# Kernel tuning notes

Hardware: AMD Instinct MI355X
Metric: run time of the kernel (lower is better)

## Reference

```python
import jax, jax.numpy as jnp
from jax import lax
import numpy as np

INPUT_SIZE = 512
HIDDEN_SIZE = 1024
OUTPUT_SIZE = 128
B, T = 64, 512


def setup_inputs() -> dict:
    key = jax.random.key(0)
    ks = jax.random.split(key, 7)
    s = 1.0 / np.sqrt(HIDDEN_SIZE)  # PyTorch LSTM init scale
    x = jax.random.normal(ks[0], (B, T, INPUT_SIZE), dtype=jnp.float32)
    W_ih = jax.random.uniform(ks[1], (4 * HIDDEN_SIZE, INPUT_SIZE), jnp.float32, -s, s)
    W_hh = jax.random.uniform(ks[2], (4 * HIDDEN_SIZE, HIDDEN_SIZE), jnp.float32, -s, s)
    b_ih = jax.random.uniform(ks[3], (4 * HIDDEN_SIZE,), jnp.float32, -s, s)
    b_hh = jax.random.uniform(ks[4], (4 * HIDDEN_SIZE,), jnp.float32, -s, s)
    W_clf = jax.random.uniform(ks[5], (OUTPUT_SIZE, HIDDEN_SIZE), jnp.float32, -s, s)
    b_clf = jax.random.uniform(ks[6], (OUTPUT_SIZE,), jnp.float32, -s, s)
    return {"x": x, "W_ih": W_ih, "W_hh": W_hh, "b_ih": b_ih,
            "b_hh": b_hh, "W_clf": W_clf, "b_clf": b_clf}


def reference(x, W_ih, W_hh, b_ih, b_hh, W_clf, b_clf):
    # Single-layer unidirectional LSTM, PyTorch gate order (i, f, g, o).
    # recurrent_dropout p=0.0 -> identity, omitted.
    Bsz = x.shape[0]
    H = W_hh.shape[1]
    h0 = jnp.zeros((Bsz, H), dtype=x.dtype)
    c0 = jnp.zeros((Bsz, H), dtype=x.dtype)
    b = b_ih + b_hh

    def step(carry, xt):
        h, c = carry
        gates = xt @ W_ih.T + h @ W_hh.T + b  # [B, 4H]
        i, f, g, o = jnp.split(gates, 4, axis=-1)
        c = jax.nn.sigmoid(f) * c + jax.nn.sigmoid(i) * jnp.tanh(g)
        h = jax.nn.sigmoid(o) * jnp.tanh(c)
        return (h, c), None

    (h_last, _), _ = lax.scan(step, (h0, c0), jnp.swapaxes(x, 0, 1))  # scan over T
    return h_last @ W_clf.T + b_clf  # [B, output_size]
```

## Files before the change

### kernel.cpp

```cpp
#include <hip/hip_runtime.h>

#define TSEQ 512
#define BATCH 64
#define INS 512
#define HID 1024
#define NOUT 128
#define NWG 256
#define NTHR 256
#define SLOT_HALFS 65536
#define BG_HALFS 32768
#define FLAGS_BYTES 32768
#define XH_OFF ((size_t)32768)
#define XH_HALFS (2ull * TSEQ * 16384)
#define WIHB_OFF (XH_OFF + XH_HALFS * 2)
#define WIHB_HALFS (128ull * 16384)
#define WHHB_OFF (WIHB_OFF + WIHB_HALFS * 2)
#define WHHB_HALFS (128ull * 32768)
#define HB_OFF_PRE (WHHB_OFF + WHHB_HALFS * 2)

typedef _Float16 half8 __attribute__((ext_vector_type(8)));
typedef float f32x4 __attribute__((ext_vector_type(4)));

__device__ __forceinline__ float sigf(float v) {
  return __builtin_amdgcn_rcpf(1.0f + __expf(-v));
}
__device__ __forceinline__ float tanh_fast(float v) {
  float e = __expf(2.0f * fabsf(v));
  float t = 1.0f - 2.0f * __builtin_amdgcn_rcpf(e + 1.0f);
  return copysignf(t, v);
}
__device__ __forceinline__ half8 cvt8(const float* p) {
  float4 lo = *(const float4*)p, hi = *(const float4*)(p + 4);
  return half8{(_Float16)lo.x, (_Float16)lo.y, (_Float16)lo.z, (_Float16)lo.w,
               (_Float16)hi.x, (_Float16)hi.y, (_Float16)hi.z, (_Float16)hi.w};
}
__device__ __forceinline__ void gload_lds16(const void* g, void* l) {
  __builtin_amdgcn_global_load_lds(
      (const __attribute__((address_space(1))) unsigned int*)g,
      (__attribute__((address_space(3))) unsigned int*)l, 16, 0, 0);
}

__global__ __launch_bounds__(NTHR, 1) void lstm_persist(
    const float* __restrict__ x, const float* __restrict__ W_ih,
    const float* __restrict__ W_hh, const float* __restrict__ b_ih,
    const float* __restrict__ b_hh, const float* __restrict__ W_clf,
    const float* __restrict__ b_clf, float* __restrict__ out,
    void* ws, int nbuf, int use_pre, int do_fence) {
  __shared__ __align__(16) char smem[65536];
  _Float16* hs = (_Float16*)smem;
  float* gates = (float*)smem;

  const int tid = threadIdx.x;
  const int wg = blockIdx.x;
  const int bg = wg >> 7;
  const int cgrp = wg & 127;
  const int wv = tid >> 6;
  const int mi = wv >> 1;
  const int ni = wv & 1;
  const int lane = tid & 63;
  const int nn = lane & 15;
  const int kq = lane >> 4;

  unsigned* flags = (unsigned*)ws;
  _Float16* xh = (_Float16*)((char*)ws + XH_OFF);
  _Float16* wihb = (_Float16*)((char*)ws + WIHB_OFF);
  _Float16* whhb = (_Float16*)((char*)ws + WHHB_OFF);
  _Float16* hb = (_Float16*)((char*)ws + (use_pre ? HB_OFF_PRE : (size_t)FLAGS_BYTES));

  __builtin_amdgcn_fence(__ATOMIC_ACQUIRE, "agent");

  const int c_l = 16 * ni + nn;
  const int ncol = (c_l >> 3) * HID + 8 * cgrp + (c_l & 7);

  if (use_pre) {
    const int gtid = wg * NTHR + tid;
    for (unsigned u = gtid; u < 2097152u; u += NWG * NTHR) {
      int ko = u & 63, t = (u >> 6) & (TSEQ - 1), b = u >> 15;
      half8 v = cvt8(x + ((size_t)b * TSEQ + t) * INS + ko * 8);
      size_t d = ((size_t)((b >> 5) * TSEQ + t) << 14) +
                 (size_t)(((((b >> 4) & 1) * 16 + (ko >> 2)) * 512) +
                          ((ko & 3) * 16 + (b & 15)) * 8);
      *(half8*)(xh + d) = v;
    }
    for (unsigned u = gtid; u < 262144u; u += NWG * NTHR) {
      int le = u & 63, kc = (u >> 6) & 15, nie = (u >> 10) & 1, cge = u >> 11;
      int c = nie * 16 + (le & 15);
      int nc = (c >> 3) * HID + 8 * cge + (c & 7);
      half8 v = cvt8(W_ih + (size_t)nc * INS + kc * 32 + (le >> 4) * 8);
      *(half8*)(wihb + (((size_t)cge << 14) + (size_t)((nie * 16 + kc) * 512 + le * 8))) = v;
    }
    for (unsigned u = gtid; u < 524288u; u += NWG * NTHR) {
      int le = u & 63, kc = (u >> 6) & 31, nie = (u >> 11) & 1, cge = u >> 12;
      int c = nie * 16 + (le & 15);
      int nc = (c >> 3) * HID + 8 * cge + (c & 7);
      half8 v = cvt8(W_hh + (size_t)nc * HID + kc * 32 + (le >> 4) * 8);
      *(half8*)(whhb + (((size_t)cge << 15) + (size_t)((nie * 32 + kc) * 512 + le * 8))) = v;
    }
    __builtin_amdgcn_fence(__ATOMIC_RELEASE, "agent");
  }

  const int dl = tid & 7, blp = tid >> 3;
  const int dgl = 8 * cgrp + dl;
  const float bI = b_ih[dgl] + b_hh[dgl];
  const float bF = b_ih[HID + dgl] + b_hh[HID + dgl];
  const float bG = b_ih[2 * HID + dgl] + b_hh[2 * HID + dgl];
  const float bO = b_ih[3 * HID + dgl] + b_hh[3 * HID + dgl];

  __syncthreads();
  if (tid == 0)
    __hip_atomic_store(flags + wg, 1u, __ATOMIC_RELAXED, __HIP_MEMORY_SCOPE_AGENT);
  {
    int ok;
    do {
      unsigned v = __hip_atomic_load(flags + tid, __ATOMIC_RELAXED,
                                     __HIP_MEMORY_SCOPE_AGENT);
      ok = (v >= 1u);
      if (!ok) __builtin_amdgcn_s_sleep(1);
    } while (!__syncthreads_and(ok));
  }
  __builtin_amdgcn_fence(__ATOMIC_ACQUIRE, "workgroup");

  auto xpart = [&](int t) -> f32x4 {
    f32x4 a0 = {0.f, 0.f, 0.f, 0.f}, a1 = {0.f, 0.f, 0.f, 0.f};
    if (use_pre) {
      const _Float16* xb = xh + ((size_t)(bg * TSEQ + t) << 14) + mi * 16 * 512 + lane * 8;
      const _Float16* wb = wihb + ((size_t)cgrp << 14) + ni * 16 * 512 + lane * 8;
#pragma unroll
      for (int kc = 0; kc < 16; kc += 2) {
        half8 A0 = *(const half8*)(xb + kc * 512);
        half8 B0 = *(const half8*)(wb + kc * 512);
        half8 A1 = *(const half8*)(xb + (kc + 1) * 512);
        half8 B1 = *(const half8*)(wb + (kc + 1) * 512);
        a0 = __builtin_amdgcn_mfma_f32_16x16x32_f16(A0, B0, a0, 0, 0, 0);
        a1 = __builtin_amdgcn_mfma_f32_16x16x32_f16(A1, B1, a1, 0, 0, 0);
      }
    } else {
      const float* xr = x + ((size_t)(32 * bg + 16 * mi + nn) * TSEQ + t) * INS + kq * 8;
      const float* wr = W_ih + (size_t)ncol * INS + kq * 8;
#pragma unroll
      for (int kc = 0; kc < 16; kc += 2) {
        half8 A0 = cvt8(xr + kc * 32), B0 = cvt8(wr + kc * 32);
        half8 A1 = cvt8(xr + (kc + 1) * 32), B1 = cvt8(wr + (kc + 1) * 32);
        a0 = __builtin_amdgcn_mfma_f32_16x16x32_f16(A0, B0, a0, 0, 0, 0);
        a1 = __builtin_amdgcn_mfma_f32_16x16x32_f16(A1, B1, a1, 0, 0, 0);
      }
    }
    return a0 + a1;
  };

  f32x4 accx = xpart(0);
  float c_state = 0.f;
  int sr = 0;

  for (int t = 0; t < TSEQ; ++t) {
    int sw = sr + 1; if (sw == nbuf) sw = 0;

    {
      const _Float16* hsrc = hb + (size_t)sr * SLOT_HALFS + (size_t)bg * BG_HALFS +
                             wv * 8192 + lane * 8;
      char* ldst = smem + (size_t)wv * 16384;
#pragma unroll
      for (int i = 0; i < 16; ++i)
        gload_lds16(hsrc + i * 512, ldst + i * 1024);
    }
    __syncthreads();

    f32x4 a0 = accx, a1 = {0.f, 0.f, 0.f, 0.f};
    {
      const _Float16* wc = whhb + ((size_t)cgrp << 15) + ni * 32 * 512 + lane * 8;
      const _Float16* ab = hs + mi * 32 * 512 + lane * 8;
#pragma unroll
      for (int kc = 0; kc < 32; kc += 2) {
        half8 A0 = *(const half8*)(ab + kc * 512);
        half8 B0 = *(const half8*)(wc + kc * 512);
        half8 A1 = *(const half8*)(ab + (kc + 1) * 512);
        half8 B1 = *(const half8*)(wc + (kc + 1) * 512);
        a0 = __builtin_amdgcn_mfma_f32_16x16x32_f16(A0, B0, a0, 0, 0, 0);
        a1 = __builtin_amdgcn_mfma_f32_16x16x32_f16(A1, B1, a1, 0, 0, 0);
      }
    }
    f32x4 acc = a0 + a1;
    __syncthreads();

    {
      int gx = c_l >> 3, dx = c_l & 7, bx = mi * 16 + kq * 4;
#pragma unroll
      for (int r = 0; r < 4; ++r) gates[(gx * 32 + bx + r) * 9 + dx] = acc[r];
    }
    __syncthreads();

    float xi = gates[(0 * 32 + blp) * 9 + dl] + bI;
    float xf = gates[(1 * 32 + blp) * 9 + dl] + bF;
    float xg = gates[(2 * 32 + blp) * 9 + dl] + bG;
    float xo = gates[(3 * 32 + blp) * 9 + dl] + bO;
    float cn = sigf(xf) * c_state + sigf(xi) * tanh_fast(xg);
    c_state = cn;
    float hv = sigf(xo) * tanh_fast(cn);

    {
      unsigned hw = (unsigned)__builtin_bit_cast(unsigned short, (_Float16)hv);
      unsigned o1 = __shfl_down(hw, 1), o2 = __shfl_down(hw, 2), o3 = __shfl_down(hw, 3);
      if ((dl & 3) == 0) {
        unsigned lo = hw | (o1 << 16), hi2 = o2 | (o3 << 16);
        unsigned long long u = ((unsigned long long)hi2 << 32) | lo;
        _Float16* hd = hb + (size_t)sw * SLOT_HALFS + (size_t)bg * BG_HALFS;
        size_t idx = (size_t)(((blp >> 4) * 32 + (cgrp >> 2)) * 512) +
                     (size_t)(((cgrp & 3) * 16 + (blp & 15)) * 8 + (dl & 4));
        __hip_atomic_store((unsigned long long*)(hd + idx), u, __ATOMIC_RELAXED,
                           __HIP_MEMORY_SCOPE_AGENT);
      }
    }

    __syncthreads();
    if (tid == 0)
      __hip_atomic_store(flags + wg, (unsigned)(t + 2), __ATOMIC_RELAXED,
                         __HIP_MEMORY_SCOPE_AGENT);

    int tn = t + 1 < TSEQ ? t + 1 : t;
    accx = xpart(tn);

    {
      const unsigned T = (unsigned)(t + 2);
      int ok;
      do {
        int okl = 1;
        if (tid < 128) {
          unsigned v = __hip_atomic_load(flags + bg * 128 + tid, __ATOMIC_RELAXED,
                                         __HIP_MEMORY_SCOPE_AGENT);
          okl = (v >= T);
        }
        ok = okl;
        if (!ok) __builtin_amdgcn_s_sleep(1);
      } while (!__syncthreads_and(ok));
    }
    __builtin_amdgcn_fence(__ATOMIC_ACQUIRE, "workgroup");
    if (do_fence) __builtin_amdgcn_fence(__ATOMIC_ACQUIRE, "agent");
    sr = sw;
  }

  {
    const _Float16* hf = hb + (size_t)sr * SLOT_HALFS + (size_t)bg * BG_HALFS;
    int bl = cgrp >> 2;
    int b = 32 * bg + bl;
    int o = (cgrp & 3) * 32 + (tid >> 3);
    int ks = tid & 7;
    int mif = bl >> 4, ml = bl & 15;
    const float* wr = W_clf + (size_t)o * HID;
    float s = 0.f;
    for (int i = 0; i < 128; ++i) {
      size_t idx = (size_t)((mif * 32 + (i >> 2)) * 512) +
                   (size_t)(((i & 3) * 16 + ml) * 8 + ks);
      s += (float)hf[idx] * wr[8 * i + ks];
    }
    s += __shfl_down(s, 4, 8);
    s += __shfl_down(s, 2, 8);
    s += __shfl_down(s, 1, 8);
    if (ks == 0) out[b * NOUT + o] = s + b_clf[o];
  }
}

extern "C" void kernel_launch(void* const* d_in, const int* in_sizes, int n_in,
                              void* d_out, int out_size, void* d_ws, size_t ws_size,
                              hipStream_t stream) {
  const float* x = (const float*)d_in[0];
  const float* W_ih = (const float*)d_in[1];
  const float* W_hh = (const float*)d_in[2];
  const float* b_ih = (const float*)d_in[3];
  const float* b_hh = (const float*)d_in[4];
  const float* W_clf = (const float*)d_in[5];
  const float* b_clf = (const float*)d_in[6];
  float* out = (float*)d_out;

  int use_pre = (ws_size >= HB_OFF_PRE + 2ull * SLOT_HALFS * 2) ? 1 : 0;
  size_t hb_off = use_pre ? HB_OFF_PRE : (size_t)FLAGS_BYTES;
  int nbuf = (ws_size >= hb_off + 129ull * SLOT_HALFS * 2) ? 129 : 2;
  int do_fence = (nbuf == 2) ? 1 : 0;

  hipMemsetAsync(d_ws, 0, FLAGS_BYTES, stream);
  hipMemsetAsync((char*)d_ws + hb_off, 0, SLOT_HALFS * 2, stream);

  void* args[] = {(void*)&x,    (void*)&W_ih,  (void*)&W_hh,   (void*)&b_ih,
                  (void*)&b_hh, (void*)&W_clf, (void*)&b_clf,  (void*)&out,
                  (void*)&d_ws, (void*)&nbuf,  (void*)&use_pre, (void*)&do_fence};
  hipLaunchCooperativeKernel((const void*)lstm_persist, dim3(NWG), dim3(NTHR),
                             args, 0, stream);
}
```

Baseline: 2.343 ms.

## Interleave gate columns so LSTM cell update runs in registers via bpermute

```diff
diff --git a/kernel.cpp b/kernel.cpp
--- a/kernel.cpp
+++ b/kernel.cpp
@@ -39,6 +39,10 @@
       (const __attribute__((address_space(1))) unsigned int*)g,
       (__attribute__((address_space(3))) unsigned int*)l, 16, 0, 0);
 }
+__device__ __forceinline__ float bperm_f(int byteaddr, float v) {
+  return __builtin_bit_cast(
+      float, __builtin_amdgcn_ds_bpermute(byteaddr, __builtin_bit_cast(int, v)));
+}
 
 __global__ __launch_bounds__(NTHR, 1) void lstm_persist(
     const float* __restrict__ x, const float* __restrict__ W_ih,
@@ -48,7 +52,6 @@
     void* ws, int nbuf, int use_pre, int do_fence) {
   __shared__ __align__(16) char smem[65536];
   _Float16* hs = (_Float16*)smem;
-  float* gates = (float*)smem;
 
   const int tid = threadIdx.x;
   const int wg = blockIdx.x;
@@ -70,7 +73,9 @@
   __builtin_amdgcn_fence(__ATOMIC_ACQUIRE, "agent");
 
   const int c_l = 16 * ni + nn;
-  const int ncol = (c_l >> 3) * HID + 8 * cgrp + (c_l & 7);
+  const int g_l = c_l & 3;
+  const int dloc = c_l >> 2;
+  const int ncol = g_l * HID + 8 * cgrp + dloc;
 
   if (use_pre) {
     const int gtid = wg * NTHR + tid;
@@ -85,39 +90,30 @@
     for (unsigned u = gtid; u < 262144u; u += NWG * NTHR) {
       int le = u & 63, kc = (u >> 6) & 15, nie = (u >> 10) & 1, cge = u >> 11;
       int c = nie * 16 + (le & 15);
-      int nc = (c >> 3) * HID + 8 * cge + (c & 7);
+      int nc = (c & 3) * HID + 8 * cge + (c >> 2);
       half8 v = cvt8(W_ih + (size_t)nc * INS + kc * 32 + (le >> 4) * 8);
       *(half8*)(wihb + (((size_t)cge << 14) + (size_t)((nie * 16 + kc) * 512 + le * 8))) = v;
     }
     for (unsigned u = gtid; u < 524288u; u += NWG * NTHR) {
       int le = u & 63, kc = (u >> 6) & 31, nie = (u >> 11) & 1, cge = u >> 12;
       int c = nie * 16 + (le & 15);
-      int nc = (c >> 3) * HID + 8 * cge + (c & 7);
+      int nc = (c & 3) * HID + 8 * cge + (c >> 2);
       half8 v = cvt8(W_hh + (size_t)nc * HID + kc * 32 + (le >> 4) * 8);
       *(half8*)(whhb + (((size_t)cge << 15) + (size_t)((nie * 32 + kc) * 512 + le * 8))) = v;
     }
     __builtin_amdgcn_fence(__ATOMIC_RELEASE, "agent");
   }
 
-  const int dl = tid & 7, blp = tid >> 3;
-  const int dgl = 8 * cgrp + dl;
-  const float bI = b_ih[dgl] + b_hh[dgl];
-  const float bF = b_ih[HID + dgl] + b_hh[HID + dgl];
-  const float bG = b_ih[2 * HID + dgl] + b_hh[2 * HID + dgl];
-  const float bO = b_ih[3 * HID + dgl] + b_hh[3 * HID + dgl];
+  const int dgl = 8 * cgrp + dloc;
+  const float b_own = b_ih[g_l * HID + dgl] + b_hh[g_l * HID + dgl];
 
   __syncthreads();
   if (tid == 0)
     __hip_atomic_store(flags + wg, 1u, __ATOMIC_RELAXED, __HIP_MEMORY_SCOPE_AGENT);
-  {
-    int ok;
-    do {
-      unsigned v = __hip_atomic_load(flags + tid, __ATOMIC_RELAXED,
-                                     __HIP_MEMORY_SCOPE_AGENT);
-      ok = (v >= 1u);
-      if (!ok) __builtin_amdgcn_s_sleep(1);
-    } while (!__syncthreads_and(ok));
-  }
+  while (__hip_atomic_load(flags + tid, __ATOMIC_RELAXED,
+                           __HIP_MEMORY_SCOPE_AGENT) < 1u)
+    __builtin_amdgcn_s_sleep(1);
+  __syncthreads();
   __builtin_amdgcn_fence(__ATOMIC_ACQUIRE, "workgroup");
 
   auto xpart = [&](int t) -> f32x4 {
@@ -149,7 +145,7 @@
   };
 
   f32x4 accx = xpart(0);
-  float c_state = 0.f;
+  f32x4 c_state = {0.f, 0.f, 0.f, 0.f};
   int sr = 0;
 
   for (int t = 0; t < TSEQ; ++t) {
@@ -180,58 +176,54 @@
       }
     }
     f32x4 acc = a0 + a1;
-    __syncthreads();
-
-    {
-      int gx = c_l >> 3, dx = c_l & 7, bx = mi * 16 + kq * 4;
-#pragma unroll
-      for (int r = 0; r < 4; ++r) gates[(gx * 32 + bx + r) * 9 + dx] = acc[r];
-    }
-    __syncthreads();
-
-    float xi = gates[(0 * 32 + blp) * 9 + dl] + bI;
-    float xf = gates[(1 * 32 + blp) * 9 + dl] + bF;
-    float xg = gates[(2 * 32 + blp) * 9 + dl] + bG;
-    float xo = gates[(3 * 32 + blp) * 9 + dl] + bO;
-    float cn = sigf(xf) * c_state + sigf(xi) * tanh_fast(xg);
-    c_state = cn;
-    float hv = sigf(xo) * tanh_fast(cn);
-
-    {
-      unsigned hw = (unsigned)__builtin_bit_cast(unsigned short, (_Float16)hv);
-      unsigned o1 = __shfl_down(hw, 1), o2 = __shfl_down(hw, 2), o3 = __shfl_down(hw, 3);
-      if ((dl & 3) == 0) {
-        unsigned lo = hw | (o1 << 16), hi2 = o2 | (o3 << 16);
+
+#pragma unroll
+    for (int r = 0; r < 4; ++r) acc[r] += b_own;
+    {
+      const int pbase = (lane & ~3) << 2;
+      f32x4 hvs;
+#pragma unroll
+      for (int r = 0; r < 4; ++r) {
+        float xi = bperm_f(pbase, acc[r]);
+        float xf = bperm_f(pbase + 4, acc[r]);
+        float xg = bperm_f(pbase + 8, acc[r]);
+        float xo = bperm_f(pbase + 12, acc[r]);
+        float cn = sigf(xf) * c_state[r] + sigf(xi) * tanh_fast(xg);
+        c_state[r] = cn;
+        hvs[r] = sigf(xo) * tanh_fast(cn);
+      }
+      float hp = g_l == 0 ? hvs[0] : g_l == 1 ? hvs[1] : g_l == 2 ? hvs[2] : hvs[3];
+      unsigned hw = (unsigned)__builtin_bit_cast(unsigned short, (_Float16)hp);
+      unsigned v4 = (unsigned)__shfl_xor((int)hw, 4);
+      unsigned v8 = (unsigned)__shfl_xor((int)hw, 8);
+      unsigned v12 = (unsigned)__shfl_xor((int)hw, 12);
+      if (nn < 4) {
+        unsigned lo = (hw & 0xffffu) | (v4 << 16);
+        unsigned hi2 = (v8 & 0xffffu) | (v12 << 16);
         unsigned long long u = ((unsigned long long)hi2 << 32) | lo;
         _Float16* hd = hb + (size_t)sw * SLOT_HALFS + (size_t)bg * BG_HALFS;
-        size_t idx = (size_t)(((blp >> 4) * 32 + (cgrp >> 2)) * 512) +
-                     (size_t)(((cgrp & 3) * 16 + (blp & 15)) * 8 + (dl & 4));
+        size_t idx = (size_t)((mi * 32 + (cgrp >> 2)) * 512) +
+                     (size_t)(((cgrp & 3) * 16 + kq * 4 + nn) * 8 + 4 * ni);
         __hip_atomic_store((unsigned long long*)(hd + idx), u, __ATOMIC_RELAXED,
                            __HIP_MEMORY_SCOPE_AGENT);
       }
     }
+
+    int tn = t + 1 < TSEQ ? t + 1 : t;
+    accx = xpart(tn);
 
     __syncthreads();
     if (tid == 0)
       __hip_atomic_store(flags + wg, (unsigned)(t + 2), __ATOMIC_RELAXED,
                          __HIP_MEMORY_SCOPE_AGENT);
-
-    int tn = t + 1 < TSEQ ? t + 1 : t;
-    accx = xpart(tn);
-
     {
       const unsigned T = (unsigned)(t + 2);
-      int ok;
-      do {
-        int okl = 1;
-        if (tid < 128) {
-          unsigned v = __hip_atomic_load(flags + bg * 128 + tid, __ATOMIC_RELAXED,
-                                         __HIP_MEMORY_SCOPE_AGENT);
-          okl = (v >= T);
-        }
-        ok = okl;
-        if (!ok) __builtin_amdgcn_s_sleep(1);
-      } while (!__syncthreads_and(ok));
+      if (tid < 128) {
+        while (__hip_atomic_load(flags + bg * 128 + tid, __ATOMIC_RELAXED,
+                                 __HIP_MEMORY_SCOPE_AGENT) < T)
+          __builtin_amdgcn_s_sleep(1);
+      }
+      __syncthreads();
     }
     __builtin_amdgcn_fence(__ATOMIC_ACQUIRE, "workgroup");
     if (do_fence) __builtin_amdgcn_fence(__ATOMIC_ACQUIRE, "agent");
```

Result: slower. 4.539 ms (+93.7%).
